# Performance work log

Hardware: AMD Instinct MI355X
Metric: run time of the kernel (lower is better)

The kernel has to match this reference:

```python
import jax, jax.numpy as jnp
import numpy as np
from jax import lax

N_EMBD = 1024
N_HEAD = 16
HEAD_DIM = N_EMBD // N_HEAD
EPS = 1e-6
B, T = 4, 2048


def setup_inputs() -> dict:
    key = jax.random.key(0)
    ks = jax.random.split(key, 5)
    scale = 1.0 / np.sqrt(N_EMBD)
    return {
        "x": jax.random.normal(ks[0], (B, T, N_EMBD), jnp.float32),
        "W_attn": jax.random.normal(ks[1], (N_EMBD, 3 * N_EMBD), jnp.float32) * scale,
        "b_attn": jax.random.normal(ks[2], (3 * N_EMBD,), jnp.float32) * 0.01,
        "W_proj": jax.random.normal(ks[3], (N_EMBD, N_EMBD), jnp.float32) * scale,
        "b_proj": jax.random.normal(ks[4], (N_EMBD,), jnp.float32) * 0.01,
    }


def _feature_map(x):
    # ELU + 1 for non-negativity
    return jax.nn.elu(x) + 1.0


def reference(x, W_attn, b_attn, W_proj, b_proj):
    Bb, Tt, C = x.shape
    qkv = x @ W_attn + b_attn  # (B,T,3C)
    q, k, v = jnp.split(qkv, 3, axis=-1)

    def to_heads(t):
        # (B,T,C) -> (T,B,H,d): scan axis leading
        return t.reshape(Bb, Tt, N_HEAD, HEAD_DIM).transpose(1, 0, 2, 3)

    q = _feature_map(to_heads(q))
    k = _feature_map(to_heads(k))
    v = to_heads(v)

    # Causal linear attention: O(d^2) running state instead of the torch
    # code's materialized (B,H,T,d,d) cumsum — same math.
    def step(carry, inp):
        kv, ksum = carry  # (B,H,d,d), (B,H,d)
        qt, kt, vt = inp  # each (B,H,d)
        kv = kv + kt[..., :, None] * vt[..., None, :]
        ksum = ksum + kt
        num = jnp.einsum('bhi,bhij->bhj', qt, kv)
        den = jnp.einsum('bhi,bhi->bh', qt, ksum)[..., None] + EPS
        return (kv, ksum), num / den

    init = (
        jnp.zeros((Bb, N_HEAD, HEAD_DIM, HEAD_DIM), x.dtype),
        jnp.zeros((Bb, N_HEAD, HEAD_DIM), x.dtype),
    )
    _, y = lax.scan(step, init, (q, k, v))  # (T,B,H,d)
    y = y.transpose(1, 0, 2, 3).reshape(Bb, Tt, C)
    return y @ W_proj + b_proj  # dropout is identity in eval mode
```

## Files before the change

kernel.cpp:

```cpp
#include <hip/hip_runtime.h>
#include <math.h>

#define BB   4
#define TT   2048
#define CC   1024
#define HH   16
#define DD   64
#define MM   (BB*TT)
#define NQKV (3*CC)
#define LCH  128
#define NCH  (TT/LCH)
#define EPSF 1e-6f

#define QKST 72
#define PST  136
#define VTST 136

typedef __bf16 bf16x8 __attribute__((ext_vector_type(8)));
typedef float  floatx4 __attribute__((ext_vector_type(4)));

__device__ __forceinline__ unsigned short f2bf(float f) {
  union { float f; unsigned int u; } v; v.f = f;
  unsigned int r = v.u + 0x7fffu + ((v.u >> 16) & 1u);
  return (unsigned short)(r >> 16);
}
__device__ __forceinline__ float bf2f(unsigned short s) {
  union { unsigned int u; float f; } v; v.u = ((unsigned int)s) << 16;
  return v.f;
}
__device__ __forceinline__ float featmap(float v) {
  return v > 0.f ? v + 1.f : __expf(v);
}
__device__ __forceinline__ void gld_lds_b128(const unsigned short* g, unsigned short* l) {
  __builtin_amdgcn_global_load_lds(
      (const __attribute__((address_space(1))) unsigned int*)g,
      (__attribute__((address_space(3))) unsigned int*)l, 16, 0, 0);
}

__device__ __forceinline__ void transpose_cvt_body(const float* __restrict__ W,
                                                   unsigned short* __restrict__ out,
                                                   int R, int Cc, int bx32, int by32, int tid) {
  __shared__ float tile[32][33];
  int tx = tid & 31, ty = tid >> 5;
  int bx = bx32 * 32, by = by32 * 32;
  #pragma unroll
  for (int i = ty; i < 32; i += 8)
    tile[i][tx] = W[(size_t)(by + i) * Cc + bx + tx];
  __syncthreads();
  #pragma unroll
  for (int i = ty; i < 32; i += 8)
    out[(size_t)(bx + i) * R + by + tx] = f2bf(tile[tx][i]);
}

__global__ __launch_bounds__(256) void prep_kernel(
    const float* __restrict__ x, unsigned short* __restrict__ xb,
    const float* __restrict__ Wa, unsigned short* __restrict__ WaT,
    const float* __restrict__ Wp, unsigned short* __restrict__ WpT) {
  int blk = blockIdx.x, tid = threadIdx.x;
  if (blk < 8192) {
    int i = (blk * 256 + tid) * 4;
    float4 f = *(const float4*)(x + i);
    ushort4 o;
    o.x = f2bf(f.x); o.y = f2bf(f.y); o.z = f2bf(f.z); o.w = f2bf(f.w);
    *(ushort4*)(xb + i) = o;
  } else if (blk < 8192 + 3072) {
    int t = blk - 8192;
    transpose_cvt_body(Wa, WaT, CC, NQKV, t % 96, t / 96, tid);
  } else {
    int t = blk - 11264;
    transpose_cvt_body(Wp, WpT, CC, CC, t % 32, t / 32, tid);
  }
}

#define GEMM_K_LOOP(A_, Bt_, K_)                                                 \
  __shared__ __align__(16) unsigned short As[128 * 64];                          \
  __shared__ __align__(16) unsigned short Bs[128 * 64];                          \
  int tid = threadIdx.x;                                                         \
  int wave = tid >> 6, lane = tid & 63;                                          \
  int lr = lane & 15, lq = lane >> 4;                                            \
  int m0 = blockIdx.y * 128, n0 = blockIdx.x * 128;                              \
  int wm = (wave >> 1) * 64, wn = (wave & 1) * 64;                               \
  int lrow = lane >> 3;                        \
  int lk = (lane & 7) ^ lrow;                       \
  int rbase = wave * 32;                                                         \
  const unsigned short* gA = A_ + (size_t)(m0 + rbase + lrow) * K_ + lk * 8;     \
  const unsigned short* gB = Bt_ + (size_t)(n0 + rbase + lrow) * K_ + lk * 8;    \
  unsigned short* lA = As + rbase * 64;                                          \
  unsigned short* lB = Bs + rbase * 64;                                          \
  floatx4 acc[4][4] = {};                                                        \
  for (int k0 = 0; k0 < K_; k0 += 64) {                                          \
    __syncthreads();                 \
    _Pragma("unroll")                                                            \
    for (int g = 0; g < 4; g++) {                                                \
      gld_lds_b128(gA + k0 + (size_t)g * 8 * K_, lA + g * 512);                  \
      gld_lds_b128(gB + k0 + (size_t)g * 8 * K_, lB + g * 512);                  \
    }                                                                            \
    __syncthreads();                                    \
    _Pragma("unroll")                                                            \
    for (int kk = 0; kk < 2; kk++) {                                             \
      bf16x8 an[4], bm[4];                                                       \
      _Pragma("unroll")                                                          \
      for (int i = 0; i < 4; i++)                                                \
        an[i] = *(const bf16x8*)&Bs[(wn + i * 16 + lr) * 64 + ((((kk << 2) + lq) ^ (lr & 7)) << 3)]; \
      _Pragma("unroll")                                                          \
      for (int j = 0; j < 4; j++)                                                \
        bm[j] = *(const bf16x8*)&As[(wm + j * 16 + lr) * 64 + ((((kk << 2) + lq) ^ (lr & 7)) << 3)]; \
      _Pragma("unroll")                                                          \
      for (int i = 0; i < 4; i++)                                                \
        _Pragma("unroll")                                                        \
        for (int j = 0; j < 4; j++)                                              \
          acc[i][j] = __builtin_amdgcn_mfma_f32_16x16x32_bf16(an[i], bm[j], acc[i][j], 0, 0, 0); \
    }                                                                            \
  }

#define BKQ   32
#define ASLT  (256 * BKQ)
#define BSLT  (192 * BKQ)
#define NT_Q  (CC / BKQ)

__global__ __launch_bounds__(512, 2) void gemm_qkv_kernel(
    const unsigned short* __restrict__ A, const unsigned short* __restrict__ Bt,
    const float* __restrict__ bias,
    unsigned short* __restrict__ qh, unsigned short* __restrict__ kh,
    unsigned short* __restrict__ vh) {
  extern __shared__ __align__(16) unsigned short lds[];
  unsigned short* Ar = lds;
  unsigned short* Br = lds + 4 * ASLT;

  const int tid = threadIdx.x;
  const int wave = tid >> 6, lane = tid & 63;
  const int lr = lane & 15, lq = lane >> 4;
  const int m0 = blockIdx.y * 256, n0 = blockIdx.x * 192;
  const int wm = (wave >> 2) * 128, wn = (wave & 3) * 48;

  const int srow = wave * 16 + (lane >> 2);
  const int cs = (lane & 3) ^ ((lane >> 3) & 3);
  const unsigned short* gA0 = A  + (size_t)(m0 + srow) * CC + cs * 8;
  const unsigned short* gB0 = Bt + (size_t)(n0 + srow) * CC + cs * 8;
  unsigned short* const stA = Ar + wave * 512;
  unsigned short* const stB = Br + wave * 512;
  const bool bhi = (wave < 4);

  const int chunk = lq ^ ((lr >> 1) & 3);
  const int roA = (wm + lr) * BKQ + chunk * 8;
  const int roB = (wn + lr) * BKQ + chunk * 8;

  floatx4 acc[3][8] = {};

#define QSTAGE_A(tt) do {                                      \
    const unsigned short* g_ = gA0 + (tt) * BKQ;               \
    unsigned short* d_ = stA + ((tt) & 3) * ASLT;              \
    gld_lds_b128(g_, d_);                                      \
    gld_lds_b128(g_ + (size_t)128 * CC, d_ + 4096);            \
  } while (0)
#define QSTAGE_B(tt) do {                                      \
    const unsigned short* g_ = gB0 + (tt) * BKQ;               \
    unsigned short* d_ = stB + ((tt) & 3) * BSLT;              \
    gld_lds_b128(g_, d_);                                      \
    if (bhi) gld_lds_b128(g_ + (size_t)128 * CC, d_ + 4096);   \
  } while (0)

  QSTAGE_A(0); QSTAGE_B(0);
  QSTAGE_A(1); QSTAGE_B(1);
  QSTAGE_A(2); QSTAGE_B(2);
  asm volatile("s_waitcnt vmcnt(6)" ::: "memory");
  __builtin_amdgcn_s_barrier();

  #pragma unroll 4
  for (int t = 0; t < NT_Q; ++t) {
    const unsigned short* sA = Ar + (t & 3) * ASLT + roA;
    const unsigned short* sB = Br + (t & 3) * BSLT + roB;
    bf16x8 an[3], bm[8];
    #pragma unroll
    for (int i = 0; i < 3; i++) an[i] = *(const bf16x8*)(sB + i * (16 * BKQ));
    #pragma unroll
    for (int j = 0; j < 8; j++) bm[j] = *(const bf16x8*)(sA + j * (16 * BKQ));
    if (t < NT_Q - 3) { QSTAGE_A(t + 3); QSTAGE_B(t + 3); }
    __builtin_amdgcn_s_barrier();
    asm volatile("s_waitcnt lgkmcnt(0)" ::: "memory");
    __builtin_amdgcn_s_setprio(1);
    #pragma unroll
    for (int i = 0; i < 3; i++)
      #pragma unroll
      for (int j = 0; j < 8; j++)
        acc[i][j] = __builtin_amdgcn_mfma_f32_16x16x32_bf16(an[i], bm[j], acc[i][j], 0, 0, 0);
    __builtin_amdgcn_s_setprio(0);
    if (t < NT_Q - 3)        asm volatile("s_waitcnt vmcnt(6)" ::: "memory");
    else if (t == NT_Q - 3)  asm volatile("s_waitcnt vmcnt(3)" ::: "memory");
    else if (t == NT_Q - 2)  asm volatile("s_waitcnt vmcnt(0)" ::: "memory");
    __builtin_amdgcn_s_barrier();
  }
#undef QSTAGE_A
#undef QSTAGE_B

  unsigned short* dstv[3];
  size_t qoff[3];
  float4 bi[3];
  bool feat[3];
  #pragma unroll
  for (int i = 0; i < 3; i++) {
    const int n = n0 + wn + i * 16 + lq * 4;
    dstv[i] = (n < 1024) ? qh : (n < 2048) ? kh : vh;
    feat[i] = (n < 2048);
    const int h = (n & 1023) >> 6, dd = n & 63;
    qoff[i] = (size_t)h * (TT * DD) + dd;
    bi[i] = *(const float4*)&bias[n];
  }
  #pragma unroll
  for (int j = 0; j < 8; j++) {
    const int m = m0 + wm + j * 16 + lr;
    const int b = m >> 11, tg = m & 2047;
    const size_t pj = (size_t)b * (HH * TT * DD) + (size_t)tg * DD;
    #pragma unroll
    for (int i = 0; i < 3; i++) {
      float v0 = acc[i][j][0] + bi[i].x, v1 = acc[i][j][1] + bi[i].y;
      float v2 = acc[i][j][2] + bi[i].z, v3 = acc[i][j][3] + bi[i].w;
      if (feat[i]) { v0 = featmap(v0); v1 = featmap(v1); v2 = featmap(v2); v3 = featmap(v3); }
      ushort4 o; o.x = f2bf(v0); o.y = f2bf(v1); o.z = f2bf(v2); o.w = f2bf(v3);
      *(ushort4*)&dstv[i][pj + qoff[i]] = o;
    }
  }
}

__global__ __launch_bounds__(256) void gemm_proj_kernel(
    const unsigned short* __restrict__ A, const unsigned short* __restrict__ Bt,
    const float* __restrict__ bias, float* __restrict__ out) {
  GEMM_K_LOOP(A, Bt, CC)
  #pragma unroll
  for (int i = 0; i < 4; i++) {
    int n = n0 + wn + i * 16 + lq * 4;
    float4 bi = *(const float4*)&bias[n];
    #pragma unroll
    for (int j = 0; j < 4; j++) {
      int m = m0 + wm + j * 16 + lr;
      float4 o;
      o.x = acc[i][j][0] + bi.x; o.y = acc[i][j][1] + bi.y;
      o.z = acc[i][j][2] + bi.z; o.w = acc[i][j][3] + bi.w;
      *(float4*)&out[(size_t)m * CC + n] = o;
    }
  }
}

__global__ __launch_bounds__(256) void chunk_state_kernel(
    const unsigned short* __restrict__ kh, const unsigned short* __restrict__ vh,
    float* __restrict__ KVx) {
  __shared__ __align__(16) unsigned short Kt[64 * VTST];
  __shared__ __align__(16) unsigned short Vt[80 * VTST];
  int blk = blockIdx.x;
  int bh = blk / NCH, c = blk % NCH;
  int tid = threadIdx.x;
  const unsigned short* kp = kh + ((size_t)bh * TT + c * LCH) * DD;
  const unsigned short* vp = vh + ((size_t)bh * TT + c * LCH) * DD;
  {
    int t = tid & 127;
    for (int j8 = (tid >> 7) * 8; j8 < DD; j8 += 16) {
      union { uint4 u; unsigned short s[8]; } wk, wv;
      wk.u = *(const uint4*)&kp[(size_t)t * DD + j8];
      wv.u = *(const uint4*)&vp[(size_t)t * DD + j8];
      #pragma unroll
      for (int jj = 0; jj < 8; jj++) {
        Kt[(j8 + jj) * VTST + t] = wk.s[jj];
        Vt[(j8 + jj) * VTST + t] = wv.s[jj];
      }
    }
  }
  for (int e = tid; e < 16 * 128; e += 256) {
    int rr = e >> 7, n = e & 127;
    Vt[(64 + rr) * VTST + n] = (rr == 0) ? (unsigned short)0x3F80 : (unsigned short)0;
  }
  __syncthreads();
  int wave = tid >> 6, lane = tid & 63;
  int lr = lane & 15, lq = lane >> 4;
  int i0 = wave * 16;
  floatx4 acc[5] = {};
  #pragma unroll
  for (int kk = 0; kk < 4; kk++) {
    bf16x8 a = *(const bf16x8*)&Kt[(i0 + lr) * VTST + kk * 32 + lq * 8];
    #pragma unroll
    for (int jt = 0; jt < 5; jt++) {
      bf16x8 b = *(const bf16x8*)&Vt[(jt * 16 + lr) * VTST + kk * 32 + lq * 8];
      acc[jt] = __builtin_amdgcn_mfma_f32_16x16x32_bf16(a, b, acc[jt], 0, 0, 0);
    }
  }
  float* o = KVx + (size_t)blk * 5120;
  #pragma unroll
  for (int jt = 0; jt < 5; jt++)
    *(float4*)&o[(jt * 16 + lr) * 64 + i0 + lq * 4] = *(float4*)&acc[jt];
}

__global__ __launch_bounds__(256) void prefix_state_kernel(const float* __restrict__ KVx,
                                                           unsigned short* __restrict__ SPb) {
  int bh = blockIdx.x / 5, jb = blockIdx.x % 5;
  int e = jb * 1024 + threadIdx.x * 4;
  size_t base0 = ((size_t)bh * NCH) * 5120 + e;
  float4 v[NCH];
  #pragma unroll
  for (int c = 0; c < NCH; c++)
    v[c] = *(const float4*)&KVx[base0 + (size_t)c * 5120];
  float r0 = 0.f, r1 = 0.f, r2 = 0.f, r3 = 0.f;
  #pragma unroll
  for (int c = 0; c < NCH; c++) {
    ushort4 o;
    o.x = f2bf(r0); o.y = f2bf(r1); o.z = f2bf(r2); o.w = f2bf(r3);
    *(ushort4*)&SPb[base0 + (size_t)c * 5120] = o;
    r0 += v[c].x; r1 += v[c].y; r2 += v[c].z; r3 += v[c].w;
  }
}

__global__ __launch_bounds__(256) void chunk_attn_kernel(
    const unsigned short* __restrict__ qh, const unsigned short* __restrict__ kh,
    const unsigned short* __restrict__ vh, const unsigned short* __restrict__ SPb,
    unsigned short* __restrict__ yb) {
  __shared__ __align__(16) unsigned short lds[128 * QKST * 2 + 80 * VTST];
  unsigned short* Qs = lds;
  unsigned short* Ks = lds + 128 * QKST;
  unsigned short* P  = lds;
  unsigned short* Vt = lds + 128 * QKST * 2;

  int blk = blockIdx.x;
  int bh = blk / NCH, c = blk % NCH;
  int b = bh / HH, h = bh % HH;
  int tid = threadIdx.x;
  const unsigned short* qp = qh + ((size_t)bh * TT + c * LCH) * DD;
  const unsigned short* kp = kh + ((size_t)bh * TT + c * LCH) * DD;
  const unsigned short* vp = vh + ((size_t)bh * TT + c * LCH) * DD;

  for (int e = tid; e < 1024; e += 256) {
    int row = e >> 3, k8 = (e & 7) * 8;
    *(uint4*)&Qs[row * QKST + k8] = *(const uint4*)&qp[(size_t)row * DD + k8];
    *(uint4*)&Ks[row * QKST + k8] = *(const uint4*)&kp[(size_t)row * DD + k8];
  }
  {
    int t = tid & 127;
    for (int j8 = (tid >> 7) * 8; j8 < DD; j8 += 16) {
      union { uint4 u; unsigned short s[8]; } w;
      w.u = *(const uint4*)&vp[(size_t)t * DD + j8];
      #pragma unroll
      for (int jj = 0; jj < 8; jj++) Vt[(j8 + jj) * VTST + t] = w.s[jj];
    }
  }
  for (int e = tid; e < 16 * 128; e += 256) {
    int rr = e >> 7, n = e & 127;
    Vt[(64 + rr) * VTST + n] = (rr == 0) ? (unsigned short)0x3F80 : (unsigned short)0;
  }
  __syncthreads();

  int wave = tid >> 6, lane = tid & 63;
  int lr = lane & 15, lq = lane >> 4;
  int mbase = wave * 32;

  bf16x8 aq[2][2];
  #pragma unroll
  for (int i = 0; i < 2; i++)
    #pragma unroll
    for (int kk = 0; kk < 2; kk++)
      aq[i][kk] = *(const bf16x8*)&Qs[(mbase + i * 16 + lr) * QKST + kk * 32 + lq * 8];

  floatx4 accT[5][2] = {};
  const unsigned short* spb = SPb + (size_t)blk * (80 * 64);
  #pragma unroll
  for (int jt = 0; jt < 5; jt++)
    #pragma unroll
    for (int kk = 0; kk < 2; kk++) {
      bf16x8 asp = *(const bf16x8*)&spb[(jt * 16 + lr) * 64 + kk * 32 + lq * 8];
      accT[jt][0] = __builtin_amdgcn_mfma_f32_16x16x32_bf16(asp, aq[0][kk], accT[jt][0], 0, 0, 0);
      accT[jt][1] = __builtin_amdgcn_mfma_f32_16x16x32_bf16(asp, aq[1][kk], accT[jt][1], 0, 0, 0);
    }
  floatx4 sacc[2][8] = {};
  #pragma unroll
  for (int nt = 0; nt < 8; nt++)
    #pragma unroll
    for (int kk = 0; kk < 2; kk++) {
      bf16x8 bk = *(const bf16x8*)&Ks[(nt * 16 + lr) * QKST + kk * 32 + lq * 8];
      sacc[0][nt] = __builtin_amdgcn_mfma_f32_16x16x32_bf16(aq[0][kk], bk, sacc[0][nt], 0, 0, 0);
      sacc[1][nt] = __builtin_amdgcn_mfma_f32_16x16x32_bf16(aq[1][kk], bk, sacc[1][nt], 0, 0, 0);
    }
  __syncthreads();

  #pragma unroll
  for (int i = 0; i < 2; i++)
    #pragma unroll
    for (int nt = 0; nt < 8; nt++) {
      int col = nt * 16 + lr;
      #pragma unroll
      for (int r = 0; r < 4; r++) {
        int m = mbase + i * 16 + lq * 4 + r;
        float v = (col <= m) ? sacc[i][nt][r] : 0.f;
        P[m * PST + col] = f2bf(v);
      }
    }
  __syncthreads();

  #pragma unroll
  for (int kk4 = 0; kk4 < 4; kk4++) {
    bf16x8 bp0 = *(const bf16x8*)&P[(mbase + lr) * PST + kk4 * 32 + lq * 8];
    bf16x8 bp1 = *(const bf16x8*)&P[(mbase + 16 + lr) * PST + kk4 * 32 + lq * 8];
    #pragma unroll
    for (int jt = 0; jt < 5; jt++) {
      bf16x8 av = *(const bf16x8*)&Vt[(jt * 16 + lr) * VTST + kk4 * 32 + lq * 8];
      accT[jt][0] = __builtin_amdgcn_mfma_f32_16x16x32_bf16(av, bp0, accT[jt][0], 0, 0, 0);
      accT[jt][1] = __builtin_amdgcn_mfma_f32_16x16x32_bf16(av, bp1, accT[jt][1], 0, 0, 0);
    }
  }

  #pragma unroll
  for (int it = 0; it < 2; it++) {
    float den = __shfl(accT[4][it][0], lr, 64);
    float inv = 1.f / (den + EPSF);
    int tg = c * LCH + mbase + it * 16 + lr;
    size_t base = ((size_t)b * TT + tg) * CC + h * DD;
    #pragma unroll
    for (int jt = 0; jt < 4; jt++) {
      ushort4 o;
      o.x = f2bf(accT[jt][it][0] * inv);
      o.y = f2bf(accT[jt][it][1] * inv);
      o.z = f2bf(accT[jt][it][2] * inv);
      o.w = f2bf(accT[jt][it][3] * inv);
      *(ushort4*)&yb[base + jt * 16 + lq * 4] = o;
    }
  }
}

extern "C" void kernel_launch(void* const* d_in, const int* in_sizes, int n_in,
                              void* d_out, int out_size, void* d_ws, size_t ws_size,
                              hipStream_t stream) {
  const float* x      = (const float*)d_in[0];
  const float* W_attn = (const float*)d_in[1];
  const float* b_attn = (const float*)d_in[2];
  const float* W_proj = (const float*)d_in[3];
  const float* b_proj = (const float*)d_in[4];
  float* out = (float*)d_out;

  char* ws = (char*)d_ws;
  size_t off = 0;
  auto alloc = [&](size_t bytes) -> char* {
    char* p = ws + off;
    off += (bytes + 255) & ~(size_t)255;
    return p;
  };
  unsigned short* xb  = (unsigned short*)alloc((size_t)MM * CC * 2);
  unsigned short* WaT = (unsigned short*)alloc((size_t)NQKV * CC * 2);
  unsigned short* WpT = (unsigned short*)alloc((size_t)CC * CC * 2);
  unsigned short* qh  = (unsigned short*)alloc((size_t)MM * CC * 2);
  unsigned short* kh  = (unsigned short*)alloc((size_t)MM * CC * 2);
  unsigned short* vh  = (unsigned short*)alloc((size_t)MM * CC * 2);
  float* KVx = (float*)alloc((size_t)BB * HH * NCH * 80 * 64 * 4);
  unsigned short* SPb = (unsigned short*)alloc((size_t)BB * HH * NCH * 80 * 64 * 2);
  unsigned short* yb = xb;

  static bool s_attr_done = false;
  if (!s_attr_done) {
    (void)hipFuncSetAttribute((const void*)gemm_qkv_kernel,
                              hipFuncAttributeMaxDynamicSharedMemorySize, 114688);
    s_attr_done = true;
  }

  prep_kernel<<<12288, 256, 0, stream>>>(x, xb, W_attn, WaT, W_proj, WpT);
  gemm_qkv_kernel<<<dim3(NQKV / 192, MM / 256), 512, 114688, stream>>>(xb, WaT, b_attn, qh, kh, vh);
  chunk_state_kernel<<<BB * HH * NCH, 256, 0, stream>>>(kh, vh, KVx);
  prefix_state_kernel<<<BB * HH * 5, 256, 0, stream>>>(KVx, SPb);
  chunk_attn_kernel<<<BB * HH * NCH, 256, 0, stream>>>(qh, kh, vh, SPb, yb);
  gemm_proj_kernel<<<dim3(CC / 128, MM / 128), 256, 0, stream>>>(yb, WpT, b_proj, out);
}
```

Baseline: 229.6 us.

## Pipeline projection GEMM with 4-stage async LDS ring; swizzle Q/K loads in attention

The projection GEMM moves from a single-buffered 128x128 tile with two barriers per 64-wide k-step to a 128x256 tile, 512 threads, and a 4-slot dynamic-LDS ring. Loads are issued three stages ahead with direct global-to-LDS copies and vmcnt waits, and MFMA runs at raised priority, so global latency overlaps with compute. The chunk attention kernel also loads Q and K straight into XOR-swizzled unpadded LDS via async loads and prefetches V into registers before the transpose store. The cost is more LDS per block (96 KB), hand-tuned wait counts that must match the issue order, and fewer blocks in the projection grid.

```diff
diff --git a/kernel.cpp b/kernel.cpp
--- a/kernel.cpp
+++ b/kernel.cpp
@@ -12,7 +12,6 @@
 #define NCH  (TT/LCH)
 #define EPSF 1e-6f
 
-#define QKST 72
 #define PST  136
 #define VTST 136
 
@@ -72,47 +71,6 @@
   }
 }
 
-#define GEMM_K_LOOP(A_, Bt_, K_)                                                 \
-  __shared__ __align__(16) unsigned short As[128 * 64];                          \
-  __shared__ __align__(16) unsigned short Bs[128 * 64];                          \
-  int tid = threadIdx.x;                                                         \
-  int wave = tid >> 6, lane = tid & 63;                                          \
-  int lr = lane & 15, lq = lane >> 4;                                            \
-  int m0 = blockIdx.y * 128, n0 = blockIdx.x * 128;                              \
-  int wm = (wave >> 1) * 64, wn = (wave & 1) * 64;                               \
-  int lrow = lane >> 3;                        \
-  int lk = (lane & 7) ^ lrow;                       \
-  int rbase = wave * 32;                                                         \
-  const unsigned short* gA = A_ + (size_t)(m0 + rbase + lrow) * K_ + lk * 8;     \
-  const unsigned short* gB = Bt_ + (size_t)(n0 + rbase + lrow) * K_ + lk * 8;    \
-  unsigned short* lA = As + rbase * 64;                                          \
-  unsigned short* lB = Bs + rbase * 64;                                          \
-  floatx4 acc[4][4] = {};                                                        \
-  for (int k0 = 0; k0 < K_; k0 += 64) {                                          \
-    __syncthreads();                 \
-    _Pragma("unroll")                                                            \
-    for (int g = 0; g < 4; g++) {                                                \
-      gld_lds_b128(gA + k0 + (size_t)g * 8 * K_, lA + g * 512);                  \
-      gld_lds_b128(gB + k0 + (size_t)g * 8 * K_, lB + g * 512);                  \
-    }                                                                            \
-    __syncthreads();                                    \
-    _Pragma("unroll")                                                            \
-    for (int kk = 0; kk < 2; kk++) {                                             \
-      bf16x8 an[4], bm[4];                                                       \
-      _Pragma("unroll")                                                          \
-      for (int i = 0; i < 4; i++)                                                \
-        an[i] = *(const bf16x8*)&Bs[(wn + i * 16 + lr) * 64 + ((((kk << 2) + lq) ^ (lr & 7)) << 3)]; \
-      _Pragma("unroll")                                                          \
-      for (int j = 0; j < 4; j++)                                                \
-        bm[j] = *(const bf16x8*)&As[(wm + j * 16 + lr) * 64 + ((((kk << 2) + lq) ^ (lr & 7)) << 3)]; \
-      _Pragma("unroll")                                                          \
-      for (int i = 0; i < 4; i++)                                                \
-        _Pragma("unroll")                                                        \
-        for (int j = 0; j < 4; j++)                                              \
-          acc[i][j] = __builtin_amdgcn_mfma_f32_16x16x32_bf16(an[i], bm[j], acc[i][j], 0, 0, 0); \
-    }                                                                            \
-  }
-
 #define BKQ   32
 #define ASLT  (256 * BKQ)
 #define BSLT  (192 * BKQ)
@@ -222,17 +180,84 @@
   }
 }
 
-__global__ __launch_bounds__(256) void gemm_proj_kernel(
+#define PBK   32
+#define PASLT (128 * PBK)
+#define PBSLT (256 * PBK)
+#define NT_P  (CC / PBK)
+
+__global__ __launch_bounds__(512, 2) void gemm_proj_kernel(
     const unsigned short* __restrict__ A, const unsigned short* __restrict__ Bt,
     const float* __restrict__ bias, float* __restrict__ out) {
-  GEMM_K_LOOP(A, Bt, CC)
+  extern __shared__ __align__(16) unsigned short lds[];
+  unsigned short* Ar = lds;
+  unsigned short* Br = lds + 4 * PASLT;
+
+  const int tid = threadIdx.x;
+  const int wave = tid >> 6, lane = tid & 63;
+  const int lr = lane & 15, lq = lane >> 4;
+  const int m0 = blockIdx.y * 128, n0 = blockIdx.x * 256;
+  const int wm = (wave >> 2) * 64, wn = (wave & 3) * 64;
+
+  const int srow = wave * 16 + (lane >> 2);
+  const int cs = (lane & 3) ^ ((lane >> 3) & 3);
+  const unsigned short* gA0 = A  + (size_t)(m0 + srow) * CC + cs * 8;
+  const unsigned short* gB0 = Bt + (size_t)(n0 + srow) * CC + cs * 8;
+  unsigned short* const stA = Ar + wave * 512;
+  unsigned short* const stB = Br + wave * 512;
+
+  const int chunk = lq ^ ((lr >> 1) & 3);
+  const int roA = (wm + lr) * PBK + chunk * 8;
+  const int roB = (wn + lr) * PBK + chunk * 8;
+
+  floatx4 acc[4][4] = {};
+
+#define PSTAGE(tt) do {                                        \
+    const unsigned short* ga_ = gA0 + (tt) * PBK;              \
+    unsigned short* da_ = stA + ((tt) & 3) * PASLT;            \
+    gld_lds_b128(ga_, da_);                                    \
+    const unsigned short* gb_ = gB0 + (tt) * PBK;              \
+    unsigned short* db_ = stB + ((tt) & 3) * PBSLT;            \
+    gld_lds_b128(gb_, db_);                                    \
+    gld_lds_b128(gb_ + (size_t)128 * CC, db_ + 4096);          \
+  } while (0)
+
+  PSTAGE(0); PSTAGE(1); PSTAGE(2);
+  asm volatile("s_waitcnt vmcnt(6)" ::: "memory");
+  __builtin_amdgcn_s_barrier();
+
+  #pragma unroll 4
+  for (int t = 0; t < NT_P; ++t) {
+    const unsigned short* sA = Ar + (t & 3) * PASLT + roA;
+    const unsigned short* sB = Br + (t & 3) * PBSLT + roB;
+    bf16x8 an[4], bm[4];
+    #pragma unroll
+    for (int i = 0; i < 4; i++) an[i] = *(const bf16x8*)(sB + i * (16 * PBK));
+    #pragma unroll
+    for (int j = 0; j < 4; j++) bm[j] = *(const bf16x8*)(sA + j * (16 * PBK));
+    if (t < NT_P - 3) PSTAGE(t + 3);
+    __builtin_amdgcn_s_barrier();
+    asm volatile("s_waitcnt lgkmcnt(0)" ::: "memory");
+    __builtin_amdgcn_s_setprio(1);
+    #pragma unroll
+    for (int i = 0; i < 4; i++)
+      #pragma unroll
+      for (int j = 0; j < 4; j++)
+        acc[i][j] = __builtin_amdgcn_mfma_f32_16x16x32_bf16(an[i], bm[j], acc[i][j], 0, 0, 0);
+    __builtin_amdgcn_s_setprio(0);
+    if (t < NT_P - 3)        asm volatile("s_waitcnt vmcnt(6)" ::: "memory");
+    else if (t == NT_P - 3)  asm volatile("s_waitcnt vmcnt(3)" ::: "memory");
+    else if (t == NT_P - 2)  asm volatile("s_waitcnt vmcnt(0)" ::: "memory");
+    __builtin_amdgcn_s_barrier();
+  }
+#undef PSTAGE
+
   #pragma unroll
   for (int i = 0; i < 4; i++) {
-    int n = n0 + wn + i * 16 + lq * 4;
-    float4 bi = *(const float4*)&bias[n];
+    const int n = n0 + wn + i * 16 + lq * 4;
+    const float4 bi = *(const float4*)&bias[n];
     #pragma unroll
     for (int j = 0; j < 4; j++) {
-      int m = m0 + wm + j * 16 + lr;
+      const int m = m0 + wm + j * 16 + lr;
       float4 o;
       o.x = acc[i][j][0] + bi.x; o.y = acc[i][j][1] + bi.y;
       o.z = acc[i][j][2] + bi.z; o.w = acc[i][j][3] + bi.w;
@@ -311,11 +336,11 @@
     const unsigned short* __restrict__ qh, const unsigned short* __restrict__ kh,
     const unsigned short* __restrict__ vh, const unsigned short* __restrict__ SPb,
     unsigned short* __restrict__ yb) {
-  __shared__ __align__(16) unsigned short lds[128 * QKST * 2 + 80 * VTST];
+  __shared__ __align__(16) unsigned short lds[17408 + 80 * VTST];
   unsigned short* Qs = lds;
-  unsigned short* Ks = lds + 128 * QKST;
+  unsigned short* Ks = lds + 8192;
   unsigned short* P  = lds;
-  unsigned short* Vt = lds + 128 * QKST * 2;
+  unsigned short* Vt = lds + 17408;
 
   int blk = blockIdx.x;
   int bh = blk / NCH, c = blk % NCH;
@@ -325,36 +350,52 @@
   const unsigned short* kp = kh + ((size_t)bh * TT + c * LCH) * DD;
   const unsigned short* vp = vh + ((size_t)bh * TT + c * LCH) * DD;
 
-  for (int e = tid; e < 1024; e += 256) {
-    int row = e >> 3, k8 = (e & 7) * 8;
-    *(uint4*)&Qs[row * QKST + k8] = *(const uint4*)&qp[(size_t)row * DD + k8];
-    *(uint4*)&Ks[row * QKST + k8] = *(const uint4*)&kp[(size_t)row * DD + k8];
-  }
+  int wave = tid >> 6, lane = tid & 63;
+  int lr = lane & 15, lq = lane >> 4;
+  int mbase = wave * 32;
+
+  const int vt = tid & 127, vj0 = (tid >> 7) * 8;
+  uint4 wv[4];
+  #pragma unroll
+  for (int ii = 0; ii < 4; ii++)
+    wv[ii] = *(const uint4*)&vp[(size_t)vt * DD + vj0 + ii * 16];
+  asm volatile("" ::: "memory");
+
   {
-    int t = tid & 127;
-    for (int j8 = (tid >> 7) * 8; j8 < DD; j8 += 16) {
-      union { uint4 u; unsigned short s[8]; } w;
-      w.u = *(const uint4*)&vp[(size_t)t * DD + j8];
-      #pragma unroll
-      for (int jj = 0; jj < 8; jj++) Vt[(j8 + jj) * VTST + t] = w.s[jj];
-    }
+    const int grow8 = lane >> 3;
+    const int gc = (lane & 7) ^ grow8;
+    const unsigned short* gq = qp + (size_t)(wave * 32 + grow8) * DD + gc * 8;
+    const unsigned short* gk = kp + (size_t)(wave * 32 + grow8) * DD + gc * 8;
+    unsigned short* dq = Qs + wave * 32 * DD;
+    unsigned short* dk = Ks + wave * 32 * DD;
+    #pragma unroll
+    for (int g = 0; g < 4; g++) {
+      gld_lds_b128(gq + (size_t)g * 8 * DD, dq + g * 512);
+      gld_lds_b128(gk + (size_t)g * 8 * DD, dk + g * 512);
+    }
+  }
+
+  #pragma unroll
+  for (int ii = 0; ii < 4; ii++) {
+    union { uint4 u; unsigned short s[8]; } w; w.u = wv[ii];
+    const int j8 = vj0 + ii * 16;
+    #pragma unroll
+    for (int jj = 0; jj < 8; jj++) Vt[(j8 + jj) * VTST + vt] = w.s[jj];
   }
   for (int e = tid; e < 16 * 128; e += 256) {
     int rr = e >> 7, n = e & 127;
     Vt[(64 + rr) * VTST + n] = (rr == 0) ? (unsigned short)0x3F80 : (unsigned short)0;
   }
+  asm volatile("s_waitcnt vmcnt(0)" ::: "memory");
   __syncthreads();
 
-  int wave = tid >> 6, lane = tid & 63;
-  int lr = lane & 15, lq = lane >> 4;
-  int mbase = wave * 32;
-
   bf16x8 aq[2][2];
   #pragma unroll
   for (int i = 0; i < 2; i++)
     #pragma unroll
     for (int kk = 0; kk < 2; kk++)
-      aq[i][kk] = *(const bf16x8*)&Qs[(mbase + i * 16 + lr) * QKST + kk * 32 + lq * 8];
+      aq[i][kk] = *(const bf16x8*)&Qs[(mbase + i * 16 + lr) * DD +
+                                      ((((kk << 2) + lq) ^ (lr & 7)) << 3)];
 
   floatx4 accT[5][2] = {};
   const unsigned short* spb = SPb + (size_t)blk * (80 * 64);
@@ -371,7 +412,8 @@
   for (int nt = 0; nt < 8; nt++)
     #pragma unroll
     for (int kk = 0; kk < 2; kk++) {
-      bf16x8 bk = *(const bf16x8*)&Ks[(nt * 16 + lr) * QKST + kk * 32 + lq * 8];
+      bf16x8 bk = *(const bf16x8*)&Ks[(nt * 16 + lr) * DD +
+                                      ((((kk << 2) + lq) ^ (lr & 7)) << 3)];
       sacc[0][nt] = __builtin_amdgcn_mfma_f32_16x16x32_bf16(aq[0][kk], bk, sacc[0][nt], 0, 0, 0);
       sacc[1][nt] = __builtin_amdgcn_mfma_f32_16x16x32_bf16(aq[1][kk], bk, sacc[1][nt], 0, 0, 0);
     }
@@ -452,6 +494,8 @@
   if (!s_attr_done) {
     (void)hipFuncSetAttribute((const void*)gemm_qkv_kernel,
                               hipFuncAttributeMaxDynamicSharedMemorySize, 114688);
+    (void)hipFuncSetAttribute((const void*)gemm_proj_kernel,
+                              hipFuncAttributeMaxDynamicSharedMemorySize, 98304);
     s_attr_done = true;
   }
 
@@ -460,5 +504,5 @@
   chunk_state_kernel<<<BB * HH * NCH, 256, 0, stream>>>(kh, vh, KVx);
   prefix_state_kernel<<<BB * HH * 5, 256, 0, stream>>>(KVx, SPb);
   chunk_attn_kernel<<<BB * HH * NCH, 256, 0, stream>>>(qh, kh, vh, SPb, yb);
-  gemm_proj_kernel<<<dim3(CC / 128, MM / 128), 256, 0, stream>>>(yb, WpT, b_proj, out);
-}
+  gemm_proj_kernel<<<dim3(CC / 256, MM / 128), 512, 98304, stream>>>(yb, WpT, b_proj, out);
+}
```

Measured after the change: 230.7 us. No clear change (+0.5%).
